# Kernel optimization log

Hardware: AMD Instinct MI355X
Metric: run time of the kernel (lower is better)

The kernel has to match this reference:

```python
import jax, jax.numpy as jnp
import numpy as np

ORDER = 2


def _masked_row_mean(v, m, safe_cnt, has_any):
    # v already zeroed outside mask; per-row mean over masked entries
    s = jnp.sum(v, axis=1, keepdims=True) / safe_cnt
    return jnp.where(has_any, s, 0.0)


def high_order_residual(x, mask, order=ORDER):
    """Vectorized faithful version of high_order_residual (braq).
    nanmean over masked entries == masked sum / count; sign/scale/shift
    are only meaningful inside the mask, outputs outside the mask are 0.
    """
    m = mask.astype(x.dtype)                       # (oc, ic)
    cnt = jnp.sum(m, axis=1, keepdims=True)        # (oc, 1)
    safe_cnt = jnp.maximum(cnt, 1.0)
    has_any = cnt > 0
    xm = x * m
    sum_order = jnp.zeros_like(x)
    for _ in range(order):
        residual = (xm - sum_order) * m            # masked residual, 0 outside
        mean = _masked_row_mean(residual, m, safe_cnt, has_any)   # (oc,1)
        centered = (residual - mean) * m           # 0 outside mask
        scale = _masked_row_mean(jnp.abs(centered), m, safe_cnt, has_any)
        binary = jnp.sign(centered) * scale + mean
        sum_order = sum_order + binary * m
    return sum_order


def setup_inputs() -> dict:
    key = jax.random.key(0)
    k1, k2 = jax.random.split(key)
    x = jax.random.normal(k1, (11008, 4096), dtype=jnp.float32) * 0.02
    mask = jax.random.randint(k2, (11008, 4096), 0, 2).astype(jnp.bool_)
    return {"x": x, "mask": mask}


def reference(x, mask):
    return high_order_residual(x, mask, ORDER)
```

## Files before the change

kernel.cpp:

```cpp
#include <hip/hip_runtime.h>
#include <stdint.h>

#define IC   4096
#define BLK  256
#define CPT  4

__device__ __forceinline__ double wsum_d(double v) {
    #pragma unroll
    for (int off = 32; off; off >>= 1) v += __shfl_xor(v, off);
    return v;
}
__device__ __forceinline__ int wsum_i(int v) {
    #pragma unroll
    for (int off = 32; off; off >>= 1) v += __shfl_xor(v, off);
    return v;
}

__global__ __launch_bounds__(BLK) void binarize_kernel(
    const float* __restrict__ x,
    const uint8_t* __restrict__ mask,
    float* __restrict__ out)
{
    __shared__ double sm_d[4];
    __shared__ int    sm_i[4];

    const int tid  = threadIdx.x;
    const int lane = tid & 63;
    const int wid  = tid >> 6;
    const int row  = blockIdx.x;

    const uint32_t probe = ((const uint32_t*)mask)[lane];
    const bool mask_is_bytes = __any(probe > 1u);

    const float* xr = x + (size_t)row * IC;

    float4 xf[CPT];
    #pragma unroll
    for (int i = 0; i < CPT; ++i)
        xf[i] = ((const float4*)xr)[i * BLK + tid];

    uint32_t bm = 0;
    if (mask_is_bytes) {
        const uint32_t* mr = (const uint32_t*)(mask + (size_t)row * IC);
        #pragma unroll
        for (int i = 0; i < CPT; ++i) {
            const uint32_t w = mr[i * BLK + tid];
            bm |= (((w * 0x01020408u) >> 24) & 0xFu) << (4 * i);
        }
    } else {
        const int4* mr = (const int4*)mask + (size_t)row * (IC / 4);
        #pragma unroll
        for (int i = 0; i < CPT; ++i) {
            int4 m4 = mr[i * BLK + tid];
            uint32_t b = (m4.x ? 1u : 0u) | (m4.y ? 2u : 0u)
                       | (m4.z ? 4u : 0u) | (m4.w ? 8u : 0u);
            bm |= b << (4 * i);
        }
    }

    double a0 = 0.0, a1 = 0.0, a2 = 0.0, a3 = 0.0;
    #pragma unroll
    for (int i = 0; i < CPT; ++i) {
        a0 += (double)(((bm >> (4*i + 0)) & 1u) ? xf[i].x : 0.0f);
        a1 += (double)(((bm >> (4*i + 1)) & 1u) ? xf[i].y : 0.0f);
        a2 += (double)(((bm >> (4*i + 2)) & 1u) ? xf[i].z : 0.0f);
        a3 += (double)(((bm >> (4*i + 3)) & 1u) ? xf[i].w : 0.0f);
    }
    {
        double sw = wsum_d((a0 + a1) + (a2 + a3));
        int    cw = wsum_i(__popc(bm));
        if (lane == 0) { sm_d[wid] = sw; sm_i[wid] = cw; }
    }
    __syncthreads();
    const double s   = (sm_d[0] + sm_d[1]) + (sm_d[2] + sm_d[3]);
    const int    cnt = (sm_i[0] + sm_i[1]) + (sm_i[2] + sm_i[3]);
    __syncthreads();

    const bool   has   = (cnt > 0);
    const double dc    = (double)(has ? cnt : 1);
    const double mean1 = has ? (s / dc) : 0.0;

    double p0 = 0.0, p1 = 0.0, p2 = 0.0, p3 = 0.0;
    int q = 0;
    #pragma unroll
    for (int i = 0; i < CPT; ++i) {
        const float e[4] = {xf[i].x, xf[i].y, xf[i].z, xf[i].w};
        {
            const bool b = (bm >> (4*i + 0)) & 1u;
            const double ce = (double)e[0] - mean1;
            p0 += b ? fabs(ce) : 0.0;
            q  += b ? (int)(ce > 0.0) - (int)(ce < 0.0) : 0;
        }
        {
            const bool b = (bm >> (4*i + 1)) & 1u;
            const double ce = (double)e[1] - mean1;
            p1 += b ? fabs(ce) : 0.0;
            q  += b ? (int)(ce > 0.0) - (int)(ce < 0.0) : 0;
        }
        {
            const bool b = (bm >> (4*i + 2)) & 1u;
            const double ce = (double)e[2] - mean1;
            p2 += b ? fabs(ce) : 0.0;
            q  += b ? (int)(ce > 0.0) - (int)(ce < 0.0) : 0;
        }
        {
            const bool b = (bm >> (4*i + 3)) & 1u;
            const double ce = (double)e[3] - mean1;
            p3 += b ? fabs(ce) : 0.0;
            q  += b ? (int)(ce > 0.0) - (int)(ce < 0.0) : 0;
        }
    }
    {
        double sw = wsum_d((p0 + p1) + (p2 + p3));
        int    qw = wsum_i(q);
        if (lane == 0) { sm_d[wid] = sw; sm_i[wid] = qw; }
    }
    __syncthreads();
    const double sa = (sm_d[0] + sm_d[1]) + (sm_d[2] + sm_d[3]);
    const int    pn = (sm_i[0] + sm_i[1]) + (sm_i[2] + sm_i[3]);
    __syncthreads();

    const double scale1 = has ? (sa / dc) : 0.0;
    const double s2    = (s - dc * mean1) - scale1 * (double)pn;
    const double mean2 = has ? (s2 / dc) : 0.0;

    const double Ap = scale1 + mean1;
    const double Am = -scale1 + mean1;
    const double A0 = mean1;

    double d0 = 0.0, d1 = 0.0, d2 = 0.0, d3 = 0.0;
    #pragma unroll
    for (int i = 0; i < CPT; ++i) {
        const float e[4] = {xf[i].x, xf[i].y, xf[i].z, xf[i].w};
        {
            const bool b = (bm >> (4*i + 0)) & 1u;
            const double xd = (double)e[0];
            const double A  = (xd > mean1) ? Ap : ((xd < mean1) ? Am : A0);
            const double c2 = (xd - A) - mean2;
            d0 += b ? fabs(c2) : 0.0;
        }
        {
            const bool b = (bm >> (4*i + 1)) & 1u;
            const double xd = (double)e[1];
            const double A  = (xd > mean1) ? Ap : ((xd < mean1) ? Am : A0);
            const double c2 = (xd - A) - mean2;
            d1 += b ? fabs(c2) : 0.0;
        }
        {
            const bool b = (bm >> (4*i + 2)) & 1u;
            const double xd = (double)e[2];
            const double A  = (xd > mean1) ? Ap : ((xd < mean1) ? Am : A0);
            const double c2 = (xd - A) - mean2;
            d2 += b ? fabs(c2) : 0.0;
        }
        {
            const bool b = (bm >> (4*i + 3)) & 1u;
            const double xd = (double)e[3];
            const double A  = (xd > mean1) ? Ap : ((xd < mean1) ? Am : A0);
            const double c2 = (xd - A) - mean2;
            d3 += b ? fabs(c2) : 0.0;
        }
    }
    {
        double sw = wsum_d((d0 + d1) + (d2 + d3));
        if (lane == 0) sm_d[wid] = sw;
    }
    __syncthreads();
    const double sd = (sm_d[0] + sm_d[1]) + (sm_d[2] + sm_d[3]);

    const double scale2 = has ? (sd / dc) : 0.0;
    const double Bp = scale2 + mean2;
    const double Bm = -scale2 + mean2;
    const double B0 = mean2;

    float* orow = out + (size_t)row * IC;
    #pragma unroll
    for (int i = 0; i < CPT; ++i) {
        const float e[4] = {xf[i].x, xf[i].y, xf[i].z, xf[i].w};
        float4 o;
        float* op = &o.x;
        #pragma unroll
        for (int k = 0; k < 4; ++k) {
            const bool b = (bm >> (4*i + k)) & 1u;
            const double xd = (double)e[k];
            const double A  = (xd > mean1) ? Ap : ((xd < mean1) ? Am : A0);
            const double c2 = (xd - A) - mean2;
            const double B  = (c2 > 0.0) ? Bp : ((c2 < 0.0) ? Bm : B0);
            const float  r  = (float)(A + B);
            op[k] = b ? r : 0.0f;
        }
        ((float4*)orow)[i * BLK + tid] = o;
    }
}

extern "C" void kernel_launch(void* const* d_in, const int* in_sizes, int n_in,
                              void* d_out, int out_size, void* d_ws, size_t ws_size,
                              hipStream_t stream) {
    const float*   x    = (const float*)d_in[0];
    const uint8_t* mask = (const uint8_t*)d_in[1];
    float*         out  = (float*)d_out;

    const int rows = in_sizes[0] / IC;
    binarize_kernel<<<rows, BLK, 0, stream>>>(x, mask, out);
}
```

Before: 403.6 us.

## Process several rows per block with register prefetch of next row

Each block now handles RPB rows in a grid-stride loop, loading the next row's x and mask into registers while the current row is reduced and written. The shared reduction slots are split into three separate regions, which removes the intermediate barriers between phases. The three divides become one reciprocal multiply. This is meant to hide memory latency and cut per-block launch and barrier overhead, at the cost of more registers (lower occupancy) and four times fewer blocks in the grid.

```diff
diff --git a/kernel.cpp b/kernel.cpp
--- a/kernel.cpp
+++ b/kernel.cpp
@@ -4,6 +4,7 @@
 #define IC   4096
 #define BLK  256
 #define CPT  4
+#define RPB  4
 
 __device__ __forceinline__ double wsum_d(double v) {
     #pragma unroll
@@ -16,48 +17,12 @@
     return v;
 }
 
-__global__ __launch_bounds__(BLK) void binarize_kernel(
-    const float* __restrict__ x,
-    const uint8_t* __restrict__ mask,
-    float* __restrict__ out)
+__device__ __forceinline__ void process_row(
+    const float4 (&xf)[CPT], const uint32_t bm,
+    float* __restrict__ orow,
+    double* sm_d, int* sm_i,
+    const int lane, const int wid, const int tid)
 {
-    __shared__ double sm_d[4];
-    __shared__ int    sm_i[4];
-
-    const int tid  = threadIdx.x;
-    const int lane = tid & 63;
-    const int wid  = tid >> 6;
-    const int row  = blockIdx.x;
-
-    const uint32_t probe = ((const uint32_t*)mask)[lane];
-    const bool mask_is_bytes = __any(probe > 1u);
-
-    const float* xr = x + (size_t)row * IC;
-
-    float4 xf[CPT];
-    #pragma unroll
-    for (int i = 0; i < CPT; ++i)
-        xf[i] = ((const float4*)xr)[i * BLK + tid];
-
-    uint32_t bm = 0;
-    if (mask_is_bytes) {
-        const uint32_t* mr = (const uint32_t*)(mask + (size_t)row * IC);
-        #pragma unroll
-        for (int i = 0; i < CPT; ++i) {
-            const uint32_t w = mr[i * BLK + tid];
-            bm |= (((w * 0x01020408u) >> 24) & 0xFu) << (4 * i);
-        }
-    } else {
-        const int4* mr = (const int4*)mask + (size_t)row * (IC / 4);
-        #pragma unroll
-        for (int i = 0; i < CPT; ++i) {
-            int4 m4 = mr[i * BLK + tid];
-            uint32_t b = (m4.x ? 1u : 0u) | (m4.y ? 2u : 0u)
-                       | (m4.z ? 4u : 0u) | (m4.w ? 8u : 0u);
-            bm |= b << (4 * i);
-        }
-    }
-
     double a0 = 0.0, a1 = 0.0, a2 = 0.0, a3 = 0.0;
     #pragma unroll
     for (int i = 0; i < CPT; ++i) {
@@ -74,11 +39,11 @@
     __syncthreads();
     const double s   = (sm_d[0] + sm_d[1]) + (sm_d[2] + sm_d[3]);
     const int    cnt = (sm_i[0] + sm_i[1]) + (sm_i[2] + sm_i[3]);
-    __syncthreads();
 
     const bool   has   = (cnt > 0);
     const double dc    = (double)(has ? cnt : 1);
-    const double mean1 = has ? (s / dc) : 0.0;
+    const double inv   = 1.0 / dc;
+    const double mean1 = has ? s * inv : 0.0;
 
     double p0 = 0.0, p1 = 0.0, p2 = 0.0, p3 = 0.0;
     int q = 0;
@@ -113,16 +78,15 @@
     {
         double sw = wsum_d((p0 + p1) + (p2 + p3));
         int    qw = wsum_i(q);
-        if (lane == 0) { sm_d[wid] = sw; sm_i[wid] = qw; }
+        if (lane == 0) { sm_d[4 + wid] = sw; sm_i[4 + wid] = qw; }
     }
     __syncthreads();
-    const double sa = (sm_d[0] + sm_d[1]) + (sm_d[2] + sm_d[3]);
-    const int    pn = (sm_i[0] + sm_i[1]) + (sm_i[2] + sm_i[3]);
-    __syncthreads();
-
-    const double scale1 = has ? (sa / dc) : 0.0;
+    const double sa = (sm_d[4] + sm_d[5]) + (sm_d[6] + sm_d[7]);
+    const int    pn = (sm_i[4] + sm_i[5]) + (sm_i[6] + sm_i[7]);
+
+    const double scale1 = has ? sa * inv : 0.0;
     const double s2    = (s - dc * mean1) - scale1 * (double)pn;
-    const double mean2 = has ? (s2 / dc) : 0.0;
+    const double mean2 = has ? s2 * inv : 0.0;
 
     const double Ap = scale1 + mean1;
     const double Am = -scale1 + mean1;
@@ -163,17 +127,16 @@
     }
     {
         double sw = wsum_d((d0 + d1) + (d2 + d3));
-        if (lane == 0) sm_d[wid] = sw;
+        if (lane == 0) sm_d[8 + wid] = sw;
     }
     __syncthreads();
-    const double sd = (sm_d[0] + sm_d[1]) + (sm_d[2] + sm_d[3]);
-
-    const double scale2 = has ? (sd / dc) : 0.0;
+    const double sd = (sm_d[8] + sm_d[9]) + (sm_d[10] + sm_d[11]);
+
+    const double scale2 = has ? sd * inv : 0.0;
     const double Bp = scale2 + mean2;
     const double Bm = -scale2 + mean2;
     const double B0 = mean2;
 
-    float* orow = out + (size_t)row * IC;
     #pragma unroll
     for (int i = 0; i < CPT; ++i) {
         const float e[4] = {xf[i].x, xf[i].y, xf[i].z, xf[i].w};
@@ -193,6 +156,90 @@
     }
 }
 
+__global__ __launch_bounds__(BLK) void binarize_kernel(
+    const float* __restrict__ x,
+    const uint8_t* __restrict__ mask,
+    float* __restrict__ out,
+    const int rows)
+{
+    __shared__ double sm_d[12];
+    __shared__ int    sm_i[8];
+
+    const int tid  = threadIdx.x;
+    const int lane = tid & 63;
+    const int wid  = tid >> 6;
+    const int G    = gridDim.x;
+
+    const uint32_t probe = ((const uint32_t*)mask)[lane];
+    const bool mask_is_bytes = __any(probe > 1u);
+
+    int row = blockIdx.x;
+
+    if (mask_is_bytes) {
+        float4   xc[CPT];
+        uint32_t mc[CPT];
+        {
+            const float4*   xp = (const float4*)(x + (size_t)row * IC);
+            const uint32_t* mp = (const uint32_t*)(mask + (size_t)row * IC);
+            #pragma unroll
+            for (int i = 0; i < CPT; ++i) { xc[i] = xp[i*BLK + tid]; mc[i] = mp[i*BLK + tid]; }
+        }
+        for (int it = 0; it < RPB && row < rows; ++it) {
+            const int nrow = row + G;
+            float4   xn[CPT];
+            uint32_t mn[CPT];
+            if (nrow < rows) {
+                const float4*   xp = (const float4*)(x + (size_t)nrow * IC);
+                const uint32_t* mp = (const uint32_t*)(mask + (size_t)nrow * IC);
+                #pragma unroll
+                for (int i = 0; i < CPT; ++i) { xn[i] = xp[i*BLK + tid]; mn[i] = mp[i*BLK + tid]; }
+            }
+            uint32_t bm = 0;
+            #pragma unroll
+            for (int i = 0; i < CPT; ++i)
+                bm |= (((mc[i] * 0x01020408u) >> 24) & 0xFu) << (4 * i);
+
+            process_row(xc, bm, out + (size_t)row * IC, sm_d, sm_i, lane, wid, tid);
+
+            #pragma unroll
+            for (int i = 0; i < CPT; ++i) { xc[i] = xn[i]; mc[i] = mn[i]; }
+            row = nrow;
+        }
+    } else {
+        float4 xc[CPT];
+        {
+            const float4* xp = (const float4*)(x + (size_t)row * IC);
+            #pragma unroll
+            for (int i = 0; i < CPT; ++i) xc[i] = xp[i*BLK + tid];
+        }
+        for (int it = 0; it < RPB && row < rows; ++it) {
+            const int nrow = row + G;
+            float4 xn[CPT];
+            if (nrow < rows) {
+                const float4* xp = (const float4*)(x + (size_t)nrow * IC);
+                #pragma unroll
+                for (int i = 0; i < CPT; ++i) xn[i] = xp[i*BLK + tid];
+            }
+            uint32_t bm = 0;
+            {
+                const int4* mq = (const int4*)mask + (size_t)row * (IC / 4);
+                #pragma unroll
+                for (int i = 0; i < CPT; ++i) {
+                    int4 m4 = mq[i*BLK + tid];
+                    uint32_t b = (m4.x ? 1u : 0u) | (m4.y ? 2u : 0u)
+                               | (m4.z ? 4u : 0u) | (m4.w ? 8u : 0u);
+                    bm |= b << (4 * i);
+                }
+            }
+            process_row(xc, bm, out + (size_t)row * IC, sm_d, sm_i, lane, wid, tid);
+
+            #pragma unroll
+            for (int i = 0; i < CPT; ++i) xc[i] = xn[i];
+            row = nrow;
+        }
+    }
+}
+
 extern "C" void kernel_launch(void* const* d_in, const int* in_sizes, int n_in,
                               void* d_out, int out_size, void* d_ws, size_t ws_size,
                               hipStream_t stream) {
@@ -201,5 +248,6 @@
     float*         out  = (float*)d_out;
 
     const int rows = in_sizes[0] / IC;
-    binarize_kernel<<<rows, BLK, 0, stream>>>(x, mask, out);
-}
+    const int grid = (rows + RPB - 1) / RPB;
+    binarize_kernel<<<grid, BLK, 0, stream>>>(x, mask, out, rows);
+}
```

After: 412.2 us. 1.02x slower.
